# Performance work log

Hardware: AMD Instinct MI355X
Metric: run time of the kernel (lower is better)

Reference implementation:

```python
import jax, jax.numpy as jnp
import numpy as np

B, S, D = 2, 4096, 1024
H, HD = 16, 64
M = 512              # memseqlen == chunk size
L = 2 * M            # memory + chunk tokens
HID = 2816
EPS = 1e-5


def setup_inputs() -> dict:
    key = jax.random.key(0)
    ks = jax.random.split(key, 16)
    sc = 0.02
    return {
        "x": jax.random.normal(ks[0], (B, S, D), jnp.float32),
        "freqs_cos": jax.random.uniform(ks[1], (L, HD // 2), jnp.float32),
        "freqs_sin": jax.random.uniform(ks[2], (L, HD // 2), jnp.float32),
        "wq": jax.random.normal(ks[3], (D, D), jnp.float32) * sc,
        "wk": jax.random.normal(ks[4], (D, D), jnp.float32) * sc,
        "wv": jax.random.normal(ks[5], (D, D), jnp.float32) * sc,
        "wo": jax.random.normal(ks[6], (D, D), jnp.float32) * sc,
        "wm": jax.random.normal(ks[7], (D, D), jnp.float32) * sc,
        "wkm": jax.random.normal(ks[8], (D, D), jnp.float32) * sc,
        "wvm": jax.random.normal(ks[9], (D, D), jnp.float32) * sc,
        "w1": jax.random.normal(ks[10], (D, HID), jnp.float32) * sc,
        "w3": jax.random.normal(ks[11], (D, HID), jnp.float32) * sc,
        "w2": jax.random.normal(ks[12], (HID, D), jnp.float32) * sc,
        "ffn_norm_w": jnp.ones((D,), jnp.float32),
        "mem_norm_w": jnp.ones((D,), jnp.float32),
        "origin_mem": jnp.zeros((1, M, D), jnp.float32),
    }


def _rmsnorm(x, w):
    return x * jax.lax.rsqrt(jnp.mean(x * x, axis=-1, keepdims=True) + EPS) * w


def _rope(t, cos, sin):
    # t: (B, L, H, HD); cos/sin: (L, HD//2). Adjacent-pair complex rotation (llama2.c style).
    tr = t.reshape(*t.shape[:-1], HD // 2, 2)
    t_r, t_i = tr[..., 0], tr[..., 1]
    c = cos[None, :, None, :]
    s = sin[None, :, None, :]
    o_r = t_r * c - t_i * s
    o_i = t_r * s + t_i * c
    return jnp.stack([o_r, o_i], axis=-1).reshape(t.shape)


def reference(x, freqs_cos, freqs_sin, wq, wk, wv, wo, wm, wkm, wvm,
              w1, w2, w3, ffn_norm_w, mem_norm_w, origin_mem):
    bsz = x.shape[0]
    cos = freqs_cos[:L]
    sin = freqs_sin[:L]
    causal = jnp.tril(jnp.ones((L, L), dtype=bool))
    scale = 1.0 / jnp.sqrt(jnp.asarray(HD, x.dtype))

    def ffn(h):
        return (jax.nn.silu(h @ w1) * (h @ w3)) @ w2

    def step(om, subx):
        # token projections
        xq = (subx @ wq).reshape(bsz, M, H, HD)
        xk = (subx @ wk).reshape(bsz, M, H, HD)
        xv = (subx @ wv).reshape(bsz, M, H, HD)
        # memory glue: wm -> ffn residual -> rmsnorm
        om2 = om @ wm
        om2 = om2 + ffn(_rmsnorm(om2, ffn_norm_w))
        om2 = _rmsnorm(om2, mem_norm_w)
        # memory projections (source bug: mq is overwritten by mk; wqm unused)
        mk = (om2 @ wkm).reshape(bsz, M, H, HD)
        mv = (om2 @ wvm).reshape(bsz, M, H, HD)
        mq = mk
        q = jnp.concatenate([mq, xq], axis=1)  # (B, L, H, HD)
        k = jnp.concatenate([mk, xk], axis=1)
        v = jnp.concatenate([mv, xv], axis=1)
        q = _rope(q, cos, sin)
        k = _rope(k, cos, sin)
        # SDPA, causal over the concatenated length (n_rep == 1, repeat_kv is identity)
        qh = q.transpose(0, 2, 1, 3)
        kh = k.transpose(0, 2, 1, 3)
        vh = v.transpose(0, 2, 1, 3)
        scores = jnp.einsum('bhqd,bhkd->bhqk', qh, kh) * scale
        scores = jnp.where(causal, scores, jnp.finfo(scores.dtype).min)
        attn = jax.nn.softmax(scores, axis=-1)
        out = jnp.einsum('bhqk,bhkd->bhqd', attn, vh)
        out = out.transpose(0, 2, 1, 3).reshape(bsz, L, D)
        om_new = out[:, M:]  # token-part becomes next memory AND this chunk's output
        return om_new, om_new

    om0 = jnp.broadcast_to(origin_mem, (bsz, M, D))
    xc = x.reshape(bsz, S // M, M, D).transpose(1, 0, 2, 3)  # (n_chunks, B, M, D)
    _, outs = jax.lax.scan(step, om0, xc)
    out = outs.transpose(1, 0, 2, 3).reshape(bsz, S, D)
    return out @ wo
```

## Files before the change

kernel.cpp:

```cpp
#include <hip/hip_runtime.h>
#include <hip/hip_bf16.h>


#define D_    1024
#define H_    16
#define HD_   64
#define M_    512
#define L_    1024
#define HID_  2816
#define NSTEP 8

typedef __hip_bfloat16 bf16;
typedef _Float16 f16;
typedef __attribute__((ext_vector_type(8))) short short8;
typedef __attribute__((ext_vector_type(8))) _Float16 f16x8;
typedef __attribute__((ext_vector_type(2))) _Float16 f16x2;
typedef __attribute__((ext_vector_type(4))) float floatx4;

__global__ void probe_dtype(const void* x, int* flag) {
  int lane = threadIdx.x;
  unsigned short v = ((const unsigned short*)x)[2 * lane];
  int e = (v >> 7) & 0xFF;
  bool sane = (e >= 100 && e <= 140);
  unsigned long long m = __ballot(sane);
  if (lane == 0) flag[0] = (__popcll(m) >= 40) ? 1 : 0;
}

__device__ __forceinline__ float load_any(const void* p, long i, int isbf) {
  return isbf ? __bfloat162float(((const bf16*)p)[i]) : ((const float*)p)[i];
}

__global__ __launch_bounds__(256) void transpose_cast(const void* in, bf16* out,
                                                      int K, int N, const int* flagp) {
  __shared__ float tile[32][33];
  int isbf = flagp[0];
  int tx = threadIdx.x & 31, ty = threadIdx.x >> 5;
  int n = blockIdx.x * 32 + tx;
#pragma unroll
  for (int i = 0; i < 4; i++) {
    int k = blockIdx.y * 32 + ty + i * 8;
    tile[ty + i * 8][tx] = load_any(in, (long)k * N + n, isbf);
  }
  __syncthreads();
  int k2 = blockIdx.y * 32 + tx;
#pragma unroll
  for (int i = 0; i < 4; i++) {
    int n2 = blockIdx.x * 32 + ty + i * 8;
    out[(long)n2 * K + k2] = __float2bfloat16(tile[tx][ty + i * 8]);
  }
}

__global__ __launch_bounds__(256) void cast_to_bf16(const void* in, bf16* out, int n,
                                                    const int* flagp) {
  int i = blockIdx.x * 256 + threadIdx.x;
  if (i < n) out[i] = __float2bfloat16(load_any(in, i, flagp[0]));
}

__global__ __launch_bounds__(256) void cast_to_f32(const void* in, float* out, int n,
                                                   const int* flagp) {
  int i = blockIdx.x * 256 + threadIdx.x;
  if (i < n) out[i] = load_any(in, i, flagp[0]);
}

__global__ __launch_bounds__(256) void init_om(const void* in, bf16* om, const int* flagp) {
  int i = blockIdx.x * 256 + threadIdx.x;
  int rem = i & (M_ * D_ - 1);
  om[i] = __float2bfloat16(load_any(in, rem, flagp[0]));
}

__global__ __launch_bounds__(256) void gemm64(
    const bf16* __restrict__ A, const bf16* __restrict__ WT,
    void* __restrict__ out, const int* __restrict__ flagp,
    int N, int K, int out_mode) {
  __shared__ char smem[16384];
  char* aT = smem;
  char* bT = smem + 8192;
  int tid = threadIdx.x;
  int C0 = blockIdx.x * 64, R0 = blockIdx.y * 64;
  int wave = tid >> 6, lane = tid & 63;
  int wm_ = wave >> 1, wn_ = wave & 1;
  floatx4 acc[2][2] = {};

  int q0 = tid, q1 = tid + 256;
  int am0 = q0 >> 3, ac0 = q0 & 7;
  int am1 = q1 >> 3, ac1 = q1 & 7;
  long grow0 = R0 + am0, grow1 = R0 + am1;
  long bn0 = (long)(C0 + am0) * K, bn1 = (long)(C0 + am1) * K;
  int lofa0 = (am0 * 8 + (ac0 ^ (am0 & 7))) * 16;
  int lofa1 = (am1 * 8 + (ac1 ^ (am1 & 7))) * 16;

  for (int k0 = 0; k0 < K; k0 += 64) {
    uint4 va0 = *(const uint4*)(A + grow0 * K + k0 + ac0 * 8);
    uint4 va1 = *(const uint4*)(A + grow1 * K + k0 + ac1 * 8);
    uint4 vb0 = *(const uint4*)(WT + bn0 + k0 + ac0 * 8);
    uint4 vb1 = *(const uint4*)(WT + bn1 + k0 + ac1 * 8);
    __syncthreads();
    *(uint4*)(aT + lofa0) = va0;
    *(uint4*)(aT + lofa1) = va1;
    *(uint4*)(bT + lofa0) = vb0;
    *(uint4*)(bT + lofa1) = vb1;
    __syncthreads();
#pragma unroll
    for (int kki = 0; kki < 2; ++kki) {
      int cbase = kki * 4 + (lane >> 4);
      short8 af[2], bfr[2];
#pragma unroll
      for (int i = 0; i < 2; ++i) {
        int ml = wm_ * 32 + i * 16 + (lane & 15);
        af[i] = *(const short8*)(aT + (ml * 8 + (cbase ^ (ml & 7))) * 16);
        int nl = wn_ * 32 + i * 16 + (lane & 15);
        bfr[i] = *(const short8*)(bT + (nl * 8 + (cbase ^ (nl & 7))) * 16);
      }
#pragma unroll
      for (int i = 0; i < 2; ++i)
#pragma unroll
        for (int j = 0; j < 2; ++j)
          acc[i][j] = __builtin_amdgcn_mfma_f32_16x16x32_bf16(af[i], bfr[j], acc[i][j], 0, 0, 0);
    }
  }
  int isbf = flagp[0];
#pragma unroll
  for (int i = 0; i < 2; ++i)
#pragma unroll
    for (int j = 0; j < 2; ++j) {
      int row = R0 + wm_ * 32 + i * 16 + (lane >> 4) * 4;
      int col = C0 + wn_ * 32 + j * 16 + (lane & 15);
#pragma unroll
      for (int rg = 0; rg < 4; ++rg) {
        float v = acc[i][j][rg];
        long off = (long)(row + rg) * N + col;
        if (out_mode == 0) ((float*)out)[off] = v;
        else if (out_mode == 1) ((f16*)out)[off] = (f16)v;
        else {
          if (isbf) ((bf16*)out)[off] = __float2bfloat16(v);
          else ((float*)out)[off] = v;
        }
      }
    }
}

__global__ __launch_bounds__(256) void gemm128(
    const bf16* __restrict__ A, const bf16* __restrict__ WT,
    void* __restrict__ out, const int* __restrict__ flagp,
    int N, int K, int out_mode) {
  __shared__ char smem[32768];
  int tid = threadIdx.x;
  int w = tid >> 6, lane = tid & 63;
  int C0 = blockIdx.x * 128, R0 = blockIdx.y * 128;
  int wm = (w >> 1) * 64, wn = (w & 1) * 64;
  int g = lane >> 4, n16 = lane & 15;
  floatx4 acc[4][4] = {};
  int lr = lane >> 3, lc = lane & 7;

  for (int k0 = 0; k0 < K; k0 += 64) {
    __syncthreads();
#pragma unroll
    for (int i = 0; i < 4; ++i) {
      int m = w * 32 + i * 8 + lr;
      int cg = lc ^ (m & 7);
      const bf16* ga = A + (size_t)(R0 + m) * K + k0 + cg * 8;
      const bf16* gb = WT + (size_t)(C0 + m) * K + k0 + cg * 8;
      __builtin_amdgcn_global_load_lds(
          (const __attribute__((address_space(1))) void*)ga,
          (__attribute__((address_space(3))) void*)(smem + (w * 32 + i * 8) * 128),
          16, 0, 0);
      __builtin_amdgcn_global_load_lds(
          (const __attribute__((address_space(1))) void*)gb,
          (__attribute__((address_space(3))) void*)(smem + 16384 + (w * 32 + i * 8) * 128),
          16, 0, 0);
    }
    __syncthreads();
#pragma unroll
    for (int kk = 0; kk < 2; ++kk) {
      short8 af[4], bfr[4];
#pragma unroll
      for (int i = 0; i < 4; ++i) {
        int ml = wm + i * 16 + n16;
        af[i] = *(const short8*)(smem + (ml * 8 + ((kk * 4 + g) ^ (ml & 7))) * 16);
        int nl = wn + i * 16 + n16;
        bfr[i] = *(const short8*)(smem + 16384 + (nl * 8 + ((kk * 4 + g) ^ (nl & 7))) * 16);
      }
#pragma unroll
      for (int i = 0; i < 4; ++i)
#pragma unroll
        for (int j = 0; j < 4; ++j)
          acc[i][j] = __builtin_amdgcn_mfma_f32_16x16x32_bf16(af[i], bfr[j], acc[i][j], 0, 0, 0);
    }
  }
  int isbf = flagp[0];
#pragma unroll
  for (int i = 0; i < 4; ++i)
#pragma unroll
    for (int j = 0; j < 4; ++j) {
      int row = R0 + wm + i * 16 + g * 4;
      int col = C0 + wn + j * 16 + n16;
#pragma unroll
      for (int rg = 0; rg < 4; ++rg) {
        float v = acc[i][j][rg];
        long off = (long)(row + rg) * N + col;
        if (out_mode == 0) ((float*)out)[off] = v;
        else if (out_mode == 1) ((f16*)out)[off] = (f16)v;
        else {
          if (isbf) ((bf16*)out)[off] = __float2bfloat16(v);
          else ((float*)out)[off] = v;
        }
      }
    }
}

__global__ __launch_bounds__(256) void rmsnorm_cast(const float* __restrict__ X,
                                                    const float* __restrict__ Wn,
                                                    bf16* __restrict__ Y,
                                                    const float* __restrict__ Xadd) {
  int row = blockIdx.x, tid = threadIdx.x;
  const float* xr = X + (long)row * D_;
  float vals[4], ss = 0.f;
#pragma unroll
  for (int i = 0; i < 4; i++) {
    int c = tid + i * 256;
    float v = xr[c];
    if (Xadd) v += Xadd[(long)row * D_ + c];
    vals[i] = v;
    ss += v * v;
  }
#pragma unroll
  for (int off = 32; off; off >>= 1) ss += __shfl_xor(ss, off);
  __shared__ float wsum[4];
  int wv = tid >> 6, lane = tid & 63;
  if (lane == 0) wsum[wv] = ss;
  __syncthreads();
  ss = wsum[0] + wsum[1] + wsum[2] + wsum[3];
  float r = rsqrtf(ss * (1.0f / D_) + 1e-5f);
#pragma unroll
  for (int i = 0; i < 4; i++) {
    int c = tid + i * 256;
    Y[(long)row * D_ + c] = __float2bfloat16(vals[i] * r * Wn[c]);
  }
}

__global__ __launch_bounds__(256) void silu_mul_cast(const float* __restrict__ g13,
                                                     bf16* __restrict__ u) {
  int c = blockIdx.x * 256 + threadIdx.x;
  int r = blockIdx.y;
  float a = g13[(long)r * (2 * HID_) + c];
  float b = g13[(long)r * (2 * HID_) + HID_ + c];
  float s = a / (1.f + __expf(-a));
  u[(long)r * HID_ + c] = __float2bfloat16(s * b);
}

__global__ __launch_bounds__(256) void rope_x(
    const f16* __restrict__ qkv, const float* __restrict__ cosf,
    const float* __restrict__ sinf, f16* __restrict__ q_x,
    f16* __restrict__ k_x, f16* __restrict__ v_xT) {
  __shared__ f16 tile[64][72];
  int pt = blockIdx.x;
  int t = blockIdx.y;
  int bh = blockIdx.z;
  int b = bh >> 4, h = bh & 15;
  int tid = threadIdx.x;
  int i = tid & 31, p0 = tid >> 5;
  size_t slab = (size_t)t * 32 + bh;
#pragma unroll
  for (int j = 0; j < 8; ++j) {
    int pl = p0 + j * 8;
    int m = pt * 64 + pl;
    int pos = 512 + m;
    long base = ((long)b * 4096 + t * 512 + m) * 3072 + h * 64 + 2 * i;
    float c = cosf[pos * 32 + i], s = sinf[pos * 32 + i];
    float q0 = (float)qkv[base], q1 = (float)qkv[base + 1];
    f16x2 qw; qw.x = (f16)((q0 * c - q1 * s) * 0.125f);
    qw.y = (f16)((q0 * s + q1 * c) * 0.125f);
    *(f16x2*)(q_x + (slab * 512 + m) * 64 + 2 * i) = qw;
    float k0 = (float)qkv[base + 1024], k1 = (float)qkv[base + 1025];
    f16x2 kw; kw.x = (f16)(k0 * c - k1 * s); kw.y = (f16)(k0 * s + k1 * c);
    *(f16x2*)(k_x + (slab * 512 + m) * 64 + 2 * i) = kw;
    tile[2 * i][pl] = qkv[base + 2048];
    tile[2 * i + 1][pl] = qkv[base + 2049];
  }
  __syncthreads();
#pragma unroll
  for (int j = 0; j < 8; ++j) {
    int d = p0 + j * 8;
    f16x2 vv; vv.x = tile[d][2 * i]; vv.y = tile[d][2 * i + 1];
    *(f16x2*)(v_xT + (slab * 64 + d) * 512 + pt * 64 + 2 * i) = vv;
  }
}

__global__ __launch_bounds__(256) void rope_mem(
    const f16* __restrict__ mkv, const float* __restrict__ cosf,
    const float* __restrict__ sinf, f16* __restrict__ k_mem,
    f16* __restrict__ v_memT) {
  __shared__ f16 tile[64][72];
  int pt = blockIdx.x;
  int bh = blockIdx.y;
  int b = bh >> 4, h = bh & 15;
  int tid = threadIdx.x;
  int i = tid & 31, p0 = tid >> 5;
#pragma unroll
  for (int j = 0; j < 8; ++j) {
    int pl = p0 + j * 8;
    int pos = pt * 64 + pl;
    long base = ((long)(b * 512 + pos)) * 2048 + h * 64 + 2 * i;
    float c = cosf[pos * 32 + i], s = sinf[pos * 32 + i];
    float k0 = (float)mkv[base], k1 = (float)mkv[base + 1];
    f16x2 kw; kw.x = (f16)(k0 * c - k1 * s); kw.y = (f16)(k0 * s + k1 * c);
    *(f16x2*)(k_mem + ((size_t)bh * 512 + pos) * 64 + 2 * i) = kw;
    tile[2 * i][pl] = mkv[base + 1024];
    tile[2 * i + 1][pl] = mkv[base + 1025];
  }
  __syncthreads();
#pragma unroll
  for (int j = 0; j < 8; ++j) {
    int d = p0 + j * 8;
    f16x2 vv; vv.x = tile[d][2 * i]; vv.y = tile[d][2 * i + 1];
    *(f16x2*)(v_memT + ((size_t)bh * 64 + d) * 512 + pt * 64 + 2 * i) = vv;
  }
}

__global__ __launch_bounds__(256) void attn_mfma(
    const f16* __restrict__ q_x, const f16* __restrict__ k_mem,
    const f16* __restrict__ v_memT, const f16* __restrict__ k_x,
    const f16* __restrict__ v_xT, bf16* __restrict__ om_bf,
    bf16* __restrict__ outs_bf, int t) {
  __shared__ char smem[24576];
  int qt = blockIdx.x, bh = blockIdx.y;
  int tid = threadIdx.x;
  int w = tid >> 6, lane = tid & 63;
  int g = lane >> 4, n16 = lane & 15;
  int numc = 9 + qt;
  int pos = 512 + qt * 64 + w * 16 + n16;
  size_t slab = (size_t)t * 32 + bh;

  f16x8 qf[2];
  {
    const f16* qp = q_x + (slab * 512 + qt * 64 + w * 16 + n16) * 64 + g * 8;
    qf[0] = *(const f16x8*)(qp);
    qf[1] = *(const f16x8*)(qp + 32);
  }
  floatx4 O[4] = {};
  float mrun = -1e30f, lrun = 0.f;

  int id0 = tid, id1 = tid + 256;
  int r0 = id0 >> 3, c0 = id0 & 7;
  int r1 = id1 >> 3, c1 = id1 & 7;
  int lof0 = ((r0 << 3) | (c0 ^ (r0 & 7))) * 16;
  int lof1 = ((r1 << 3) | (c1 ^ (r1 & 7))) * 16;

  auto kaddr = [&](int c, int r) -> const f16* {
    return (c < 8) ? k_mem + ((size_t)bh * 512 + c * 64 + r) * 64
                   : k_x + (slab * 512 + (c - 8) * 64 + r) * 64;
  };
  auto vaddr = [&](int c, int d) -> const f16* {
    return (c < 8) ? v_memT + ((size_t)bh * 64 + d) * 512 + c * 64
                   : v_xT + (slab * 64 + d) * 512 + (c - 8) * 64;
  };

  uint4 kv0 = *(const uint4*)(kaddr(0, r0) + c0 * 8);
  uint4 kv1 = *(const uint4*)(kaddr(0, r1) + c1 * 8);
  uint4 vv0 = *(const uint4*)(vaddr(0, r0) + c0 * 8);
  uint4 vv1 = *(const uint4*)(vaddr(0, r1) + c1 * 8);

  char* Pw = smem + 16384 + w * 2048;

  for (int c = 0; c < numc; ++c) {
    __syncthreads();
    *(uint4*)(smem + lof0) = kv0;
    *(uint4*)(smem + lof1) = kv1;
    *(uint4*)(smem + 8192 + lof0) = vv0;
    *(uint4*)(smem + 8192 + lof1) = vv1;
    if (c + 1 < numc) {
      kv0 = *(const uint4*)(kaddr(c + 1, r0) + c0 * 8);
      kv1 = *(const uint4*)(kaddr(c + 1, r1) + c1 * 8);
      vv0 = *(const uint4*)(vaddr(c + 1, r0) + c0 * 8);
      vv1 = *(const uint4*)(vaddr(c + 1, r1) + c1 * 8);
    }
    __syncthreads();

    floatx4 S[4] = {};
#pragma unroll
    for (int kk = 0; kk < 2; ++kk) {
#pragma unroll
      for (int tn = 0; tn < 4; ++tn) {
        int row = tn * 16 + n16;
        f16x8 kf = *(const f16x8*)(smem + (((row << 3) | ((kk * 4 + g) ^ (row & 7))) * 16));
        S[tn] = __builtin_amdgcn_mfma_f32_16x16x32_f16(kf, qf[kk], S[tn], 0, 0, 0);
      }
    }
    if (c == numc - 1) {
      int kb = 512 + (c - 8) * 64;
#pragma unroll
      for (int tn = 0; tn < 4; ++tn)
#pragma unroll
        for (int r = 0; r < 4; ++r) {
          int key = kb + tn * 16 + g * 4 + r;
          if (key > pos) S[tn][r] = -1e30f;
        }
    }
    float smax = -1e30f;
#pragma unroll
    for (int tn = 0; tn < 4; ++tn)
#pragma unroll
      for (int r = 0; r < 4; ++r) smax = fmaxf(smax, S[tn][r]);
    smax = fmaxf(smax, __shfl_xor(smax, 16));
    smax = fmaxf(smax, __shfl_xor(smax, 32));
    float newm = fmaxf(mrun, smax);
    float corr = __expf(mrun - newm);
    mrun = newm;
    float lsum = 0.f;
    f16 pv[16];
#pragma unroll
    for (int tn = 0; tn < 4; ++tn)
#pragma unroll
      for (int r = 0; r < 4; ++r) {
        float p = __expf(S[tn][r] - newm);
        lsum += p;
        pv[tn * 4 + r] = (f16)p;
      }
    lsum += __shfl_xor(lsum, 16);
    lsum += __shfl_xor(lsum, 32);
    lrun = lrun * corr + lsum;
    float cr[4];
#pragma unroll
    for (int r = 0; r < 4; ++r) cr[r] = __shfl(corr, g * 4 + r);
#pragma unroll
    for (int dt = 0; dt < 4; ++dt)
#pragma unroll
      for (int r = 0; r < 4; ++r) O[dt][r] *= cr[r];
#pragma unroll
    for (int tn = 0; tn < 4; ++tn)
#pragma unroll
      for (int r = 0; r < 4; ++r) {
        int kap = tn * 16 + g * 4 + r;
        *(f16*)(Pw + (((n16 << 3) | ((kap >> 3) ^ (n16 & 7))) * 16 + (kap & 7) * 2)) =
            pv[tn * 4 + r];
      }
#pragma unroll
    for (int kk = 0; kk < 2; ++kk) {
      f16x8 pf = *(const f16x8*)(Pw + (((n16 << 3) | ((kk * 4 + g) ^ (n16 & 7))) * 16));
#pragma unroll
      for (int dt = 0; dt < 4; ++dt) {
        int row = dt * 16 + n16;
        f16x8 vf =
            *(const f16x8*)(smem + 8192 + (((row << 3) | ((kk * 4 + g) ^ (row & 7))) * 16));
        O[dt] = __builtin_amdgcn_mfma_f32_16x16x32_f16(pf, vf, O[dt], 0, 0, 0);
      }
    }
  }
  float rl = 1.0f / lrun;
  float rlr[4];
#pragma unroll
  for (int r = 0; r < 4; ++r) rlr[r] = __shfl(rl, g * 4 + r);
  int b = bh >> 4, h = bh & 15;
#pragma unroll
  for (int dt = 0; dt < 4; ++dt)
#pragma unroll
    for (int r = 0; r < 4; ++r) {
      int qq = qt * 64 + w * 16 + g * 4 + r;
      bf16 v = __float2bfloat16(O[dt][r] * rlr[r]);
      size_t col = h * 64 + dt * 16 + n16;
      om_bf[((size_t)(b * 512 + qq)) * 1024 + col] = v;
      outs_bf[((size_t)(b * 4096 + t * 512 + qq)) * 1024 + col] = v;
    }
}

extern "C" void kernel_launch(void* const* d_in, const int* in_sizes, int n_in,
                              void* d_out, int out_size, void* d_ws, size_t ws_size,
                              hipStream_t stream) {
  (void)in_sizes; (void)n_in; (void)out_size; (void)ws_size;
  const void* x   = d_in[0];
  const void* fc  = d_in[1];
  const void* fs  = d_in[2];
  const void* wq  = d_in[3];
  const void* wk  = d_in[4];
  const void* wv  = d_in[5];
  const void* wo  = d_in[6];
  const void* wm  = d_in[7];
  const void* wkm = d_in[8];
  const void* wvm = d_in[9];
  const void* w1  = d_in[10];
  const void* w3  = d_in[11];
  const void* w2  = d_in[12];
  const void* fnw = d_in[13];
  const void* mnw = d_in[14];
  const void* om0 = d_in[15];

  char* p = (char*)d_ws;
  auto alloc = [&](size_t bytes) -> char* {
    char* r = p;
    p += (bytes + 255) & ~(size_t)255;
    return r;
  };
  int*   flag    = (int*)alloc(256);
  bf16*  wqkvT   = (bf16*)alloc((size_t)3 * 1048576 * 2);
  bf16*  wmT     = (bf16*)alloc((size_t)1048576 * 2);
  bf16*  wkmvmT  = (bf16*)alloc((size_t)2 * 1048576 * 2);
  bf16*  w13T    = (bf16*)alloc((size_t)2 * 2883584 * 2);
  bf16*  w2T     = (bf16*)alloc((size_t)2883584 * 2);
  bf16*  woT     = (bf16*)alloc((size_t)1048576 * 2);
  bf16*  xb      = (bf16*)alloc((size_t)8388608 * 2);
  float* cosf    = (float*)alloc((size_t)32768 * 4);
  float* sinf    = (float*)alloc((size_t)32768 * 4);
  float* ffnw    = (float*)alloc((size_t)1024 * 4);
  float* memw    = (float*)alloc((size_t)1024 * 4);
  bf16*  om_bf   = (bf16*)alloc((size_t)1048576 * 2);
  bf16*  outs_bf = (bf16*)alloc((size_t)8388608 * 2);
  f16*   q_x     = (f16*)alloc((size_t)8 * 32 * 512 * 64 * 2);
  f16*   k_x     = (f16*)alloc((size_t)8 * 32 * 512 * 64 * 2);
  f16*   v_xT    = (f16*)alloc((size_t)8 * 32 * 512 * 64 * 2);
  char*  shr     = alloc((size_t)8192 * 3072 * 2);
  f16*   qkvf_all = (f16*)shr;
  char*  lp = shr;
  auto lalloc = [&](size_t bytes) -> char* {
    char* r = lp;
    lp += (bytes + 255) & ~(size_t)255;
    return r;
  };
  float* om2a   = (float*)lalloc((size_t)1048576 * 4);
  bf16*  h_bf   = (bf16*)lalloc((size_t)1048576 * 2);
  float* g13    = (float*)lalloc((size_t)5767168 * 4);
  bf16*  u_bf   = (bf16*)lalloc((size_t)2883584 * 2);
  float* fbuf   = (float*)lalloc((size_t)1048576 * 4);
  bf16*  om2_bf = (bf16*)lalloc((size_t)1048576 * 2);
  f16*   mkv    = (f16*)lalloc((size_t)2097152 * 2);
  f16*   k_mem  = (f16*)lalloc((size_t)1048576 * 2);
  f16*   v_memT = (f16*)lalloc((size_t)1048576 * 2);

  dim3 tb(256);
  probe_dtype<<<1, 64, 0, stream>>>(x, flag);

  transpose_cast<<<dim3(32, 32), tb, 0, stream>>>(wq, wqkvT, 1024, 1024, flag);
  transpose_cast<<<dim3(32, 32), tb, 0, stream>>>(wk, wqkvT + 1048576, 1024, 1024, flag);
  transpose_cast<<<dim3(32, 32), tb, 0, stream>>>(wv, wqkvT + 2 * 1048576, 1024, 1024, flag);
  transpose_cast<<<dim3(32, 32), tb, 0, stream>>>(wm, wmT, 1024, 1024, flag);
  transpose_cast<<<dim3(32, 32), tb, 0, stream>>>(wkm, wkmvmT, 1024, 1024, flag);
  transpose_cast<<<dim3(32, 32), tb, 0, stream>>>(wvm, wkmvmT + 1048576, 1024, 1024, flag);
  transpose_cast<<<dim3(88, 32), tb, 0, stream>>>(w1, w13T, 1024, 2816, flag);
  transpose_cast<<<dim3(88, 32), tb, 0, stream>>>(w3, w13T + 2883584, 1024, 2816, flag);
  transpose_cast<<<dim3(32, 88), tb, 0, stream>>>(w2, w2T, 2816, 1024, flag);
  transpose_cast<<<dim3(32, 32), tb, 0, stream>>>(wo, woT, 1024, 1024, flag);

  cast_to_bf16<<<32768, tb, 0, stream>>>(x, xb, 8388608, flag);
  cast_to_f32<<<128, tb, 0, stream>>>(fc, cosf, 32768, flag);
  cast_to_f32<<<128, tb, 0, stream>>>(fs, sinf, 32768, flag);
  cast_to_f32<<<4, tb, 0, stream>>>(fnw, ffnw, 1024, flag);
  cast_to_f32<<<4, tb, 0, stream>>>(mnw, memw, 1024, flag);
  init_om<<<4096, tb, 0, stream>>>(om0, om_bf, flag);

  gemm128<<<dim3(24, 64), tb, 0, stream>>>(xb, wqkvT, qkvf_all, flag, 3072, 1024, 1);
  rope_x<<<dim3(8, 8, 32), tb, 0, stream>>>(qkvf_all, cosf, sinf, q_x, k_x, v_xT);

  for (int t = 0; t < NSTEP; ++t) {
    gemm64<<<dim3(16, 16), tb, 0, stream>>>(om_bf, wmT, om2a, flag, 1024, 1024, 0);
    rmsnorm_cast<<<1024, tb, 0, stream>>>(om2a, ffnw, h_bf, nullptr);
    gemm128<<<dim3(44, 8), tb, 0, stream>>>(h_bf, w13T, g13, flag, 5632, 1024, 0);
    silu_mul_cast<<<dim3(11, 1024), tb, 0, stream>>>(g13, u_bf);
    gemm64<<<dim3(16, 16), tb, 0, stream>>>(u_bf, w2T, fbuf, flag, 1024, 2816, 0);
    rmsnorm_cast<<<1024, tb, 0, stream>>>(om2a, memw, om2_bf, fbuf);
    gemm64<<<dim3(32, 16), tb, 0, stream>>>(om2_bf, wkmvmT, mkv, flag, 2048, 1024, 1);
    rope_mem<<<dim3(8, 32), tb, 0, stream>>>(mkv, cosf, sinf, k_mem, v_memT);
    attn_mfma<<<dim3(8, 32), tb, 0, stream>>>(q_x, k_mem, v_memT, k_x, v_xT,
                                              om_bf, outs_bf, t);
  }
  gemm128<<<dim3(8, 64), tb, 0, stream>>>(outs_bf, woT, d_out, flag, 1024, 1024, 2);
}
```

Measured before the change: 1.276 ms.

## Fuse SiLU-mul into W1/W3 GEMM epilogue and split-K the small GEMMs

W1 and W3 rows are now interleaved in the transposed weight, so each pair of adjacent GEMM output columns holds a gate and an up value. The gemm128 epilogue can then apply SiLU-multiply through a lane shuffle and write bf16 directly, which removes the large fp32 g13 buffer and the separate silu kernel. The wm and w2 GEMMs use a new split-K-by-2 kernel that writes two partial outputs, doubling the block count for these low-occupancy shapes. The following rmsnorm sums the partials, and in one case writes the summed residual back. This adds an extra partial-buffer write and read in exchange for better parallelism.

```diff
diff --git a/kernel.cpp b/kernel.cpp
--- a/kernel.cpp
+++ b/kernel.cpp
@@ -31,7 +31,8 @@
 }
 
 __global__ __launch_bounds__(256) void transpose_cast(const void* in, bf16* out,
-                                                      int K, int N, const int* flagp) {
+                                                      int K, int N, const int* flagp,
+                                                      int stride, int off) {
   __shared__ float tile[32][33];
   int isbf = flagp[0];
   int tx = threadIdx.x & 31, ty = threadIdx.x >> 5;
@@ -46,7 +47,7 @@
 #pragma unroll
   for (int i = 0; i < 4; i++) {
     int n2 = blockIdx.x * 32 + ty + i * 8;
-    out[(long)n2 * K + k2] = __float2bfloat16(tile[tx][ty + i * 8]);
+    out[((long)n2 * stride + off) * K + k2] = __float2bfloat16(tile[tx][ty + i * 8]);
   }
 }
 
@@ -136,6 +137,71 @@
           else ((float*)out)[off] = v;
         }
       }
+    }
+}
+
+__global__ __launch_bounds__(256) void gemm64_sk(
+    const bf16* __restrict__ A, const bf16* __restrict__ WT,
+    float* __restrict__ out0, float* __restrict__ out1,
+    int N, int Kfull, int Ksplit) {
+  __shared__ char smem[16384];
+  char* aT = smem;
+  char* bT = smem + 8192;
+  int tid = threadIdx.x;
+  int C0 = blockIdx.x * 64, R0 = blockIdx.y * 64;
+  int kb = blockIdx.z;
+  float* out = kb ? out1 : out0;
+  int kbeg = kb * Ksplit, kend = kbeg + Ksplit;
+  int wave = tid >> 6, lane = tid & 63;
+  int wm_ = wave >> 1, wn_ = wave & 1;
+  floatx4 acc[2][2] = {};
+
+  int q0 = tid, q1 = tid + 256;
+  int am0 = q0 >> 3, ac0 = q0 & 7;
+  int am1 = q1 >> 3, ac1 = q1 & 7;
+  long grow0 = R0 + am0, grow1 = R0 + am1;
+  long bn0 = (long)(C0 + am0) * Kfull, bn1 = (long)(C0 + am1) * Kfull;
+  int lofa0 = (am0 * 8 + (ac0 ^ (am0 & 7))) * 16;
+  int lofa1 = (am1 * 8 + (ac1 ^ (am1 & 7))) * 16;
+
+  for (int k0 = kbeg; k0 < kend; k0 += 64) {
+    uint4 va0 = *(const uint4*)(A + grow0 * Kfull + k0 + ac0 * 8);
+    uint4 va1 = *(const uint4*)(A + grow1 * Kfull + k0 + ac1 * 8);
+    uint4 vb0 = *(const uint4*)(WT + bn0 + k0 + ac0 * 8);
+    uint4 vb1 = *(const uint4*)(WT + bn1 + k0 + ac1 * 8);
+    __syncthreads();
+    *(uint4*)(aT + lofa0) = va0;
+    *(uint4*)(aT + lofa1) = va1;
+    *(uint4*)(bT + lofa0) = vb0;
+    *(uint4*)(bT + lofa1) = vb1;
+    __syncthreads();
+#pragma unroll
+    for (int kki = 0; kki < 2; ++kki) {
+      int cbase = kki * 4 + (lane >> 4);
+      short8 af[2], bfr[2];
+#pragma unroll
+      for (int i = 0; i < 2; ++i) {
+        int ml = wm_ * 32 + i * 16 + (lane & 15);
+        af[i] = *(const short8*)(aT + (ml * 8 + (cbase ^ (ml & 7))) * 16);
+        int nl = wn_ * 32 + i * 16 + (lane & 15);
+        bfr[i] = *(const short8*)(bT + (nl * 8 + (cbase ^ (nl & 7))) * 16);
+      }
+#pragma unroll
+      for (int i = 0; i < 2; ++i)
+#pragma unroll
+        for (int j = 0; j < 2; ++j)
+          acc[i][j] = __builtin_amdgcn_mfma_f32_16x16x32_bf16(af[i], bfr[j], acc[i][j], 0, 0, 0);
+    }
+  }
+#pragma unroll
+  for (int i = 0; i < 2; ++i)
+#pragma unroll
+    for (int j = 0; j < 2; ++j) {
+      int row = R0 + wm_ * 32 + i * 16 + (lane >> 4) * 4;
+      int col = C0 + wn_ * 32 + j * 16 + (lane & 15);
+#pragma unroll
+      for (int rg = 0; rg < 4; ++rg)
+        out[(long)(row + rg) * N + col] = acc[i][j][rg];
     }
 }
 
@@ -197,6 +263,16 @@
 #pragma unroll
       for (int rg = 0; rg < 4; ++rg) {
         float v = acc[i][j][rg];
+        if (out_mode == 3) {
+          float partner = __shfl_xor(v, 1);
+          if ((n16 & 1) == 0) {
+            float a = v;
+            float s = a / (1.f + __expf(-a));
+            ((bf16*)out)[(long)(row + rg) * HID_ + (col >> 1)] =
+                __float2bfloat16(s * partner);
+          }
+          continue;
+        }
         long off = (long)(row + rg) * N + col;
         if (out_mode == 0) ((float*)out)[off] = v;
         else if (out_mode == 1) ((f16*)out)[off] = (f16)v;
@@ -211,7 +287,9 @@
 __global__ __launch_bounds__(256) void rmsnorm_cast(const float* __restrict__ X,
                                                     const float* __restrict__ Wn,
                                                     bf16* __restrict__ Y,
-                                                    const float* __restrict__ Xadd) {
+                                                    const float* __restrict__ X1,
+                                                    const float* __restrict__ X2,
+                                                    float* __restrict__ sumout) {
   int row = blockIdx.x, tid = threadIdx.x;
   const float* xr = X + (long)row * D_;
   float vals[4], ss = 0.f;
@@ -219,7 +297,8 @@
   for (int i = 0; i < 4; i++) {
     int c = tid + i * 256;
     float v = xr[c];
-    if (Xadd) v += Xadd[(long)row * D_ + c];
+    if (X1) v += X1[(long)row * D_ + c];
+    if (X2) v += X2[(long)row * D_ + c];
     vals[i] = v;
     ss += v * v;
   }
@@ -234,18 +313,9 @@
 #pragma unroll
   for (int i = 0; i < 4; i++) {
     int c = tid + i * 256;
+    if (sumout) sumout[(long)row * D_ + c] = vals[i];
     Y[(long)row * D_ + c] = __float2bfloat16(vals[i] * r * Wn[c]);
   }
-}
-
-__global__ __launch_bounds__(256) void silu_mul_cast(const float* __restrict__ g13,
-                                                     bf16* __restrict__ u) {
-  int c = blockIdx.x * 256 + threadIdx.x;
-  int r = blockIdx.y;
-  float a = g13[(long)r * (2 * HID_) + c];
-  float b = g13[(long)r * (2 * HID_) + HID_ + c];
-  float s = a / (1.f + __expf(-a));
-  u[(long)r * HID_ + c] = __float2bfloat16(s * b);
 }
 
 __global__ __launch_bounds__(256) void rope_x(
@@ -517,9 +587,9 @@
   };
   float* om2a   = (float*)lalloc((size_t)1048576 * 4);
   bf16*  h_bf   = (bf16*)lalloc((size_t)1048576 * 2);
-  float* g13    = (float*)lalloc((size_t)5767168 * 4);
   bf16*  u_bf   = (bf16*)lalloc((size_t)2883584 * 2);
   float* fbuf   = (float*)lalloc((size_t)1048576 * 4);
+  float* fbuf2  = (float*)lalloc((size_t)1048576 * 4);
   bf16*  om2_bf = (bf16*)lalloc((size_t)1048576 * 2);
   f16*   mkv    = (f16*)lalloc((size_t)2097152 * 2);
   f16*   k_mem  = (f16*)lalloc((size_t)1048576 * 2);
@@ -528,16 +598,16 @@
   dim3 tb(256);
   probe_dtype<<<1, 64, 0, stream>>>(x, flag);
 
-  transpose_cast<<<dim3(32, 32), tb, 0, stream>>>(wq, wqkvT, 1024, 1024, flag);
-  transpose_cast<<<dim3(32, 32), tb, 0, stream>>>(wk, wqkvT + 1048576, 1024, 1024, flag);
-  transpose_cast<<<dim3(32, 32), tb, 0, stream>>>(wv, wqkvT + 2 * 1048576, 1024, 1024, flag);
-  transpose_cast<<<dim3(32, 32), tb, 0, stream>>>(wm, wmT, 1024, 1024, flag);
-  transpose_cast<<<dim3(32, 32), tb, 0, stream>>>(wkm, wkmvmT, 1024, 1024, flag);
-  transpose_cast<<<dim3(32, 32), tb, 0, stream>>>(wvm, wkmvmT + 1048576, 1024, 1024, flag);
-  transpose_cast<<<dim3(88, 32), tb, 0, stream>>>(w1, w13T, 1024, 2816, flag);
-  transpose_cast<<<dim3(88, 32), tb, 0, stream>>>(w3, w13T + 2883584, 1024, 2816, flag);
-  transpose_cast<<<dim3(32, 88), tb, 0, stream>>>(w2, w2T, 2816, 1024, flag);
-  transpose_cast<<<dim3(32, 32), tb, 0, stream>>>(wo, woT, 1024, 1024, flag);
+  transpose_cast<<<dim3(32, 32), tb, 0, stream>>>(wq, wqkvT, 1024, 1024, flag, 1, 0);
+  transpose_cast<<<dim3(32, 32), tb, 0, stream>>>(wk, wqkvT + 1048576, 1024, 1024, flag, 1, 0);
+  transpose_cast<<<dim3(32, 32), tb, 0, stream>>>(wv, wqkvT + 2 * 1048576, 1024, 1024, flag, 1, 0);
+  transpose_cast<<<dim3(32, 32), tb, 0, stream>>>(wm, wmT, 1024, 1024, flag, 1, 0);
+  transpose_cast<<<dim3(32, 32), tb, 0, stream>>>(wkm, wkmvmT, 1024, 1024, flag, 1, 0);
+  transpose_cast<<<dim3(32, 32), tb, 0, stream>>>(wvm, wkmvmT + 1048576, 1024, 1024, flag, 1, 0);
+  transpose_cast<<<dim3(88, 32), tb, 0, stream>>>(w1, w13T, 1024, 2816, flag, 2, 0);
+  transpose_cast<<<dim3(88, 32), tb, 0, stream>>>(w3, w13T, 1024, 2816, flag, 2, 1);
+  transpose_cast<<<dim3(32, 88), tb, 0, stream>>>(w2, w2T, 2816, 1024, flag, 1, 0);
+  transpose_cast<<<dim3(32, 32), tb, 0, stream>>>(wo, woT, 1024, 1024, flag, 1, 0);
 
   cast_to_bf16<<<32768, tb, 0, stream>>>(x, xb, 8388608, flag);
   cast_to_f32<<<128, tb, 0, stream>>>(fc, cosf, 32768, flag);
@@ -550,12 +620,11 @@
   rope_x<<<dim3(8, 8, 32), tb, 0, stream>>>(qkvf_all, cosf, sinf, q_x, k_x, v_xT);
 
   for (int t = 0; t < NSTEP; ++t) {
-    gemm64<<<dim3(16, 16), tb, 0, stream>>>(om_bf, wmT, om2a, flag, 1024, 1024, 0);
-    rmsnorm_cast<<<1024, tb, 0, stream>>>(om2a, ffnw, h_bf, nullptr);
-    gemm128<<<dim3(44, 8), tb, 0, stream>>>(h_bf, w13T, g13, flag, 5632, 1024, 0);
-    silu_mul_cast<<<dim3(11, 1024), tb, 0, stream>>>(g13, u_bf);
-    gemm64<<<dim3(16, 16), tb, 0, stream>>>(u_bf, w2T, fbuf, flag, 1024, 2816, 0);
-    rmsnorm_cast<<<1024, tb, 0, stream>>>(om2a, memw, om2_bf, fbuf);
+    gemm64_sk<<<dim3(16, 16, 2), tb, 0, stream>>>(om_bf, wmT, om2a, fbuf, 1024, 1024, 512);
+    rmsnorm_cast<<<1024, tb, 0, stream>>>(om2a, ffnw, h_bf, fbuf, nullptr, om2a);
+    gemm128<<<dim3(44, 8), tb, 0, stream>>>(h_bf, w13T, u_bf, flag, 5632, 1024, 3);
+    gemm64_sk<<<dim3(16, 16, 2), tb, 0, stream>>>(u_bf, w2T, fbuf, fbuf2, 1024, 2816, 1408);
+    rmsnorm_cast<<<1024, tb, 0, stream>>>(om2a, memw, om2_bf, fbuf, fbuf2, nullptr);
     gemm64<<<dim3(32, 16), tb, 0, stream>>>(om2_bf, wkmvmT, mkv, flag, 2048, 1024, 1);
     rope_mem<<<dim3(8, 32), tb, 0, stream>>>(mkv, cosf, sinf, k_mem, v_memT);
     attn_mfma<<<dim3(8, 32), tb, 0, stream>>>(q_x, k_mem, v_memT, k_x, v_xT,
```

New measurement: 1.150 ms. -9.8%, faster.
